# Performance work log

Hardware: AMD Instinct MI355X
Metric: run time of the kernel (lower is better)

The kernel has to match this reference:

```python
import jax, jax.numpy as jnp
import numpy as np

HIDDEN = 64

def setup_inputs() -> dict:
    key = jax.random.key(0)
    ks = jax.random.split(key, 9)
    B, C, H, W = 32, 64, 64, 64
    h = HIDDEN
    s = 0.05
    return {
        "inputs": jax.random.normal(ks[0], (B, C, H, W), jnp.float32),
        # 1x1 Conv2d input->4h gates, stored as [4h, C]
        "w_i2s": jax.random.normal(ks[1], (4 * h, C), jnp.float32) * s,
        "b_i2s": jax.random.normal(ks[2], (4 * h,), jnp.float32) * s,
        # Conv1d(h, 4h, kernel=2): [4h, h, 2]
        "w_s2s": jax.random.normal(ks[3], (4 * h, h, 2), jnp.float32) * s,
        "b_s2s": jax.random.normal(ks[4], (4 * h,), jnp.float32) * s,
        # Conv1d(h, h, kernel=2): [h, h, 2]
        "w_c2c": jax.random.normal(ks[5], (h, h, 2), jnp.float32) * s,
        "b_c2c": jax.random.normal(ks[6], (h,), jnp.float32) * s,
        # 1x1 Conv2d h->2h upsampling, stored as [2h, h]
        "w_up": jax.random.normal(ks[7], (2 * h, h), jnp.float32) * s,
        "b_up": jax.random.normal(ks[8], (2 * h,), jnp.float32) * s,
    }


def _diagonal_lstm(inputs, w_i2s, b_i2s, w_s2s, b_s2s, w_c2c, b_c2c, w_up, b_up):
    B, C, H, W = inputs.shape
    h = w_s2s.shape[1]
    NW = H + W - 1  # skewed width

    # ---- skew: row r of the image shifted right by r columns ----
    rows = jnp.arange(H)[:, None]          # [H,1]
    cols = rows + jnp.arange(W)[None, :]   # [H,W]
    skewed = jnp.zeros((B, C, H, NW), inputs.dtype).at[:, :, rows, cols].set(inputs)

    # ---- input-to-state 1x1 conv -> [B, 4h, H, NW] ----
    i2s = jnp.einsum('bchw,oc->bohw', skewed, w_i2s) + b_i2s[None, :, None, None]
    # per-step input: [NW, B, H*4h]  (layout (H, 4h) flattened, as in torch)
    rnn_in = jnp.transpose(i2s, (3, 0, 2, 1)).reshape(NW, B, H * 4 * h)

    # conv1d(kernel=2) taps: out[p] = W0 @ state[p-1] + W1 @ state[p] (+bias)
    Ws0, Ws1 = w_s2s[:, :, 0], w_s2s[:, :, 1]
    Wc0, Wc1 = w_c2c[:, :, 0], w_c2c[:, :, 1]

    def step(carry, i2s_t):
        c_prev, h_prev = carry  # each [B, H, h]
        zrow = jnp.zeros((B, 1, h), inputs.dtype)
        h_shift = jnp.concatenate([zrow, h_prev[:, :-1]], axis=1)
        c_shift = jnp.concatenate([zrow, c_prev[:, :-1]], axis=1)
        s2s = (jnp.einsum('bph,oh->bpo', h_shift, Ws0)
               + jnp.einsum('bph,oh->bpo', h_prev, Ws1)
               + b_s2s)                       # [B, H, 4h]
        c2c = (jnp.einsum('bph,oh->bpo', c_shift, Wc0)
               + jnp.einsum('bph,oh->bpo', c_prev, Wc1)
               + b_c2c)                       # [B, H, h]
        lstm = jax.nn.sigmoid(i2s_t + s2s.reshape(B, H * 4 * h))
        ig, gg, fg, og = jnp.split(lstm, 4, axis=1)  # each [B, h*H] (faithful flat split)
        c2c_flat = c2c.reshape(B, H * h)
        c = fg * c2c_flat + ig * gg
        hh = og * jnp.tanh(c)
        new_carry = (c.reshape(B, H, h), hh.reshape(B, H, h))
        return new_carry, hh

    init = (jnp.zeros((B, H, h), inputs.dtype), jnp.zeros((B, H, h), inputs.dtype))
    _, outs = jax.lax.scan(step, init, rnn_in)   # outs: [NW, B, H*h]

    # [NW,B,H*h] -> [B, NW, H, h] -> [B, h, H, NW]
    outs = jnp.transpose(outs, (1, 0, 2)).reshape(B, NW, H, h)
    skewed_out = jnp.transpose(outs, (0, 3, 2, 1))

    # ---- unskew ----
    unskewed = skewed_out[:, :, rows, cols]  # [B, h, H, W]

    # ---- 1x1 upsampling conv h -> 2h ----
    return jnp.einsum('bchw,oc->bohw', unskewed, w_up) + b_up[None, :, None, None]


def reference(inputs, w_i2s, b_i2s, w_s2s, b_s2s, w_c2c, b_c2c, w_up, b_up):
    return _diagonal_lstm(inputs, w_i2s, b_i2s, w_s2s, b_s2s, w_c2c, b_c2c, w_up, b_up)
```

## Files before the change

### kernel.cpp

```cpp
#include <hip/hip_runtime.h>
#include <cstdint>
#include <cstddef>


typedef unsigned int u32;
typedef unsigned short u16;
typedef __bf16 bf16x8 __attribute__((ext_vector_type(8)));
typedef float f32x4 __attribute__((ext_vector_type(4)));

#define NSTEP 127
#define MFMA(a, b, c) __builtin_amdgcn_mfma_f32_16x16x32_bf16(a, b, c, 0, 0, 0)
#define LOG2E 1.4426950408889634f
#define SCL (-1.4426950408889634f)
#define T2L 2.8853900817779268f
#define RHO(r) ((((r) ^ ((r) >> 3))) & 7)

static __device__ __forceinline__ u16 f2bf(float f) {
    u32 u = __builtin_bit_cast(u32, f);
    u32 r = u + 0x7FFFu + ((u >> 16) & 1u);
    return (u16)(r >> 16);
}
static __device__ __forceinline__ u32 pack2(float a, float b) {
    return (u32)f2bf(a) | ((u32)f2bf(b) << 16);
}
static __device__ __forceinline__ float lo2f(u32 u) {
    return __builtin_bit_cast(float, u << 16);
}
static __device__ __forceinline__ float hi2f(u32 u) {
    return __builtin_bit_cast(float, u & 0xFFFF0000u);
}
static __device__ __forceinline__ float sigm2(float y) {
    return __builtin_amdgcn_rcpf(1.f + __builtin_amdgcn_exp2f(y));
}
static __device__ __forceinline__ float tanh_fast(float x) {
    float r = __builtin_amdgcn_rcpf(1.f + __builtin_amdgcn_exp2f(x * T2L));
    return __builtin_fmaf(-2.f, r, 1.f);
}

__global__ __launch_bounds__(256) void repack_w(
    const float* __restrict__ w_s2s, const float* __restrict__ w_c2c,
    const float* __restrict__ bi, const float* __restrict__ bs,
    const float* __restrict__ w_up, float* __restrict__ Wg,
    float* __restrict__ Wc, u16* __restrict__ biasRow,
    u16* __restrict__ w_upB) {
    int idx = blockIdx.x * 256 + threadIdx.x;
    if (idx < 32768) {
        int o = idx >> 7, kk = idx & 127, half = kk >> 6, k = kk & 63;
        Wg[idx] = SCL * w_s2s[(o * 64 + k) * 2 + half];
        return;
    }
    int j = idx - 32768;
    if (j < 8192) {
        int o = j >> 7, kk = j & 127, half = kk >> 6, k = kk & 63;
        Wc[j] = w_c2c[(o * 64 + k) * 2 + half];
        return;
    }
    j -= 8192;
    if (j < 256) {
        int m15 = j >> 4, nq = (j >> 2) & 3, nb = j & 3;
        int o = 64 * nq + 16 * nb + m15;
        biasRow[j] = f2bf(SCL * (bi[o] + bs[o]));
        return;
    }
    j -= 256;
    if (j < 8192) w_upB[j] = f2bf(w_up[j]);
}

__global__ __launch_bounds__(256, 2) void i2s_kernel(
    const float* __restrict__ in, const float* __restrict__ w_i2s,
    const float* __restrict__ bi, const float* __restrict__ bs,
    const u32* __restrict__ biasU32, u32* __restrict__ out_u32) {
    const int bid = blockIdx.x;
    const int b = bid >> 6, r = bid & 63;
    const int tid = threadIdx.x;
    const int lane = tid & 63;
    const int wv = __builtin_amdgcn_readfirstlane(tid >> 6);
    const int m15 = lane & 15, g4 = lane >> 4;

    __shared__ __align__(16) u32 sT[64 * 129];
    __shared__ __align__(16) u32 Xt[64 * 32];
    char* XtB = (char*)Xt;

    {
        const int w = tid & 63, cp = tid >> 6;
        const float* xp = in + (size_t)b * 262144 + r * 64 + w;
#pragma unroll
        for (int pass = 0; pass < 8; pass++) {
            int c = pass * 8 + cp * 2;
            float x0 = xp[(size_t)c * 4096];
            float x1 = xp[(size_t)(c + 1) * 4096];
            *(u32*)(XtB + ((w * 128 + c * 2) ^ ((w & 7) << 4))) = pack2(x0, x1);
        }
    }

    bf16x8 Af[4][2];
#pragma unroll
    for (int m = 0; m < 4; m++)
#pragma unroll
        for (int kt = 0; kt < 2; kt++) {
            const float* p =
                w_i2s + (wv * 64 + m * 16 + m15) * 64 + kt * 32 + g4 * 8;
            bf16x8 f;
#pragma unroll
            for (int j = 0; j < 8; j++) f[j] = (__bf16)p[j];
            Af[m][kt] = f;
        }
    float bias[4][4];
#pragma unroll
    for (int m = 0; m < 4; m++)
#pragma unroll
        for (int reg = 0; reg < 4; reg++) {
            int o = wv * 64 + m * 16 + 4 * g4 + reg;
            bias[m][reg] = bi[o] + bs[o];
        }

    __syncthreads();

    f32x4 acc[4][4] = {};
#pragma unroll
    for (int nt = 0; nt < 4; nt++) {
        const int w = nt * 16 + m15;
        bf16x8 Bf[2];
#pragma unroll
        for (int kt = 0; kt < 2; kt++)
            Bf[kt] = __builtin_bit_cast(
                bf16x8, *(const uint4*)(XtB + ((w * 128 + kt * 64 + g4 * 16) ^
                                               ((w & 7) << 4))));
#pragma unroll
        for (int m = 0; m < 4; m++)
#pragma unroll
            for (int kt = 0; kt < 2; kt++)
                acc[m][nt] = MFMA(Af[m][kt], Bf[kt], acc[m][nt]);
    }

#pragma unroll
    for (int nt = 0; nt < 4; nt++) {
        const int w = nt * 16 + m15;
#pragma unroll
        for (int reg = 0; reg < 4; reg++)
#pragma unroll
            for (int mp = 0; mp < 2; mp++) {
                float v0 = SCL * (acc[2 * mp][nt][reg] + bias[2 * mp][reg]);
                float v1 =
                    SCL * (acc[2 * mp + 1][nt][reg] + bias[2 * mp + 1][reg]);
                sT[w * 129 + (4 * g4 + reg) * 8 + wv * 2 + mp] = pack2(v0, v1);
            }
    }
    __syncthreads();

    const size_t base = ((size_t)(b * 64 + r) * 66 + 1) * 128;
#pragma unroll
    for (int loop = 0; loop < 32; loop++) {
        int idx = loop * 256 + tid;
        int w = idx >> 7, cu = idx & 127;
        out_u32[base + idx] = sT[w * 129 + cu];
    }
    if (tid < 128) {
        u32 v = biasU32[tid];
        out_u32[base - 128 + tid] = v;
        out_u32[base + 8192 + tid] = v;
    }
}

__global__ __launch_bounds__(512, 2) void scan_kernel(
    const u16* __restrict__ i2sP, const float* __restrict__ Wg,
    const float* __restrict__ Wc, const float* __restrict__ b_c2c,
    u16* __restrict__ hh16) {
    const int b = blockIdx.x;
    const int tid = threadIdx.x;
    const int lane = tid & 63;
    const int wv = __builtin_amdgcn_readfirstlane(tid >> 6);
    const int mh = wv >> 2, nq = wv & 3;
    const int mtc = wv >> 1, ktc0 = (wv & 1) * 2;
    const int m15 = lane & 15, g4 = lane >> 4;

    __shared__ __align__(16) u32 sM[10304];
    __shared__ __align__(16) u32 sCCm[2048];
    char* smB = (char*)sM;
    char* ccB = (char*)sCCm;

    for (int i = tid; i < 10304; i += 512) sM[i] = 0;

    bf16x8 BW[4][4];
    float bcc[4];
#pragma unroll
    for (int nb = 0; nb < 4; nb++) {
        int o = 64 * nq + 16 * nb + m15;
        bcc[nb] = b_c2c[16 * nb + m15];
#pragma unroll
        for (int kt = 0; kt < 4; kt++) {
            const float* p = Wg + o * 128 + kt * 32 + g4 * 8;
            bf16x8 f;
#pragma unroll
            for (int j = 0; j < 8; j++) f[j] = (__bf16)p[j];
            BW[nb][kt] = f;
        }
    }
    bf16x8 BC[2][4];
#pragma unroll
    for (int i = 0; i < 2; i++) {
        int o2 = 16 * (ktc0 + i) + m15;
#pragma unroll
        for (int kt = 0; kt < 4; kt++) {
            const float* p = Wc + o2 * 128 + kt * 32 + g4 * 8;
            bf16x8 f;
#pragma unroll
            for (int j = 0; j < 8; j++) f[j] = (__bf16)p[j];
            BC[i][kt] = f;
        }
    }

    int aG[2][4], aC[4], wOff[2][4], ccR[2][4], ccP[4], bOffB[2][4];
#pragma unroll
    for (int mi = 0; mi < 2; mi++) {
        int mt = 2 * mh + mi;
#pragma unroll
        for (int kt = 0; kt < 4; kt++) {
            int P = 16 * (m15 & 3) + 4 * mt + (m15 >> 2);
            int phys = P + (kt >> 1) - 1;
            int chunk = (kt & 1) * 4 + g4;
            aG[mi][kt] = (phys < 0) ? (32768 + chunk * 16)
                                    : (phys * 128 + ((chunk ^ RHO(phys)) * 16));
        }
        int p2 = 16 * mt + 4 * g4 + nq;
#pragma unroll
        for (int nb = 0; nb < 4; nb++) {
            int k = 16 * nb + m15;
            wOff[mi][nb] =
                8192 + p2 * 128 + (((k >> 3) ^ RHO(p2)) * 16) + (k & 7) * 2;
            int rp = p2 >> 1;
            ccR[mi][nb] = (rp * 64 + ((k + 8 * rp) & 63)) * 4;
            int prerow = 16 * nb + 4 * mt + g4;
            bOffB[mi][nb] = (prerow * 66 + 1) * 512 + 32 * m15 + 8 * nq;
        }
    }
#pragma unroll
    for (int kt = 0; kt < 4; kt++) {
        int crow = 16 * mtc + m15;
        int phys = crow + (kt >> 1) - 1;
        int chunk = (kt & 1) * 4 + g4;
        aC[kt] = (phys < 0) ? (32896 + chunk * 16)
                            : (16384 + phys * 128 + ((chunk ^ RHO(phys)) * 16));
    }
#pragma unroll
    for (int i = 0; i < 2; i++) {
        int k = 16 * (ktc0 + i) + m15;
        int rp0 = 8 * mtc + 2 * g4, rp1 = rp0 + 1;
        ccP[2 * i] = (rp0 * 64 + ((k + 8 * rp0) & 63)) * 4;
        ccP[2 * i + 1] = (rp1 * 64 + ((k + 8 * rp1) & 63)) * 4;
    }

    const char* i2sB = (const char*)i2sP + (size_t)b * (64 * 66 * 512);
    u16* hp16[2];
    int p2s[2];
#pragma unroll
    for (int mi = 0; mi < 2; mi++) {
        int p2 = 16 * (2 * mh + mi) + 4 * g4 + nq;
        p2s[mi] = p2;
        hp16[mi] = hh16 + (size_t)b * 262144 + p2 * 4032 + m15;
    }

    uint2 IV[2][4];
#pragma unroll
    for (int mi = 0; mi < 2; mi++) {
        int mt = 2 * mh + mi;
#pragma unroll
        for (int r = 0; r < 4; r++) {
            int prerow = 16 * r + 4 * mt + g4;
            int w = min(max(0 - prerow, -1), 64);
            IV[mi][r] = *(const uint2*)(i2sB + (bOffB[mi][r] + (w << 9)));
        }
    }

    u16 hbKeep[2][4];
    u16* hpPrev[2];
    bool vstPrev[2];
#pragma unroll
    for (int mi = 0; mi < 2; mi++) {
        vstPrev[mi] = false;
        hpPrev[mi] = hp16[mi];
    }

    __syncthreads();

    for (int t = 0; t < NSTEP; t++) {
#pragma unroll
        for (int mi = 0; mi < 2; mi++)
            if (vstPrev[mi]) {
#pragma unroll
                for (int nb = 0; nb < 4; nb++)
                    hpPrev[mi][nb * 16] = hbKeep[mi][nb];
            }

        uint2 IVn[2][4];
#pragma unroll
        for (int mi = 0; mi < 2; mi++) {
            int mt = 2 * mh + mi;
#pragma unroll
            for (int r = 0; r < 4; r++) {
                int prerow = 16 * r + 4 * mt + g4;
                int w = min(max(t + 1 - prerow, -1), 64);
                IVn[mi][r] = *(const uint2*)(i2sB + (bOffB[mi][r] + (w << 9)));
            }
        }

        f32x4 accG[2][4];
#pragma unroll
        for (int mi = 0; mi < 2; mi++) {
#pragma unroll
            for (int r = 0; r < 4; r++) {
                accG[mi][0][r] = lo2f(IV[mi][r].x);
                accG[mi][1][r] = hi2f(IV[mi][r].x);
                accG[mi][2][r] = lo2f(IV[mi][r].y);
                accG[mi][3][r] = hi2f(IV[mi][r].y);
            }
            bf16x8 Ag[4];
#pragma unroll
            for (int kt = 0; kt < 4; kt++)
                Ag[kt] = __builtin_bit_cast(bf16x8,
                                            *(const uint4*)(smB + aG[mi][kt]));
#pragma unroll
            for (int nb = 0; nb < 4; nb++)
#pragma unroll
                for (int kt = 0; kt < 4; kt++)
                    accG[mi][nb] = MFMA(Ag[kt], BW[nb][kt], accG[mi][nb]);
        }
        f32x4 accC[2] = {};
        {
            bf16x8 Ac[4];
#pragma unroll
            for (int kt = 0; kt < 4; kt++)
                Ac[kt] =
                    __builtin_bit_cast(bf16x8, *(const uint4*)(smB + aC[kt]));
#pragma unroll
            for (int i = 0; i < 2; i++)
#pragma unroll
                for (int kt = 0; kt < 4; kt++)
                    accC[i] = MFMA(Ac[kt], BC[i][kt], accC[i]);
        }

#pragma unroll
        for (int i = 0; i < 2; i++) {
            *(u32*)(ccB + ccP[2 * i]) = pack2(accC[i][0], accC[i][1]);
            *(u32*)(ccB + ccP[2 * i + 1]) = pack2(accC[i][2], accC[i][3]);
        }
        __syncthreads();

#pragma unroll
        for (int mi = 0; mi < 2; mi++) {
            int p2 = p2s[mi];
            bool vst = (u32)(t - p2) < 64u;
#pragma unroll
            for (int nb = 0; nb < 4; nb++) {
                u32 cw = *(const u32*)(ccB + ccR[mi][nb]);
                float cc = ((nq & 1) ? hi2f(cw) : lo2f(cw)) + bcc[nb];
                float si = sigm2(accG[mi][nb][0]);
                float sg = sigm2(accG[mi][nb][1]);
                float sf = sigm2(accG[mi][nb][2]);
                float so = sigm2(accG[mi][nb][3]);
                float c1 = __builtin_fmaf(sf, cc, si * sg);
                float h1 = so * tanh_fast(c1);
                u16 hb = f2bf(h1);
                *(u16*)(smB + wOff[mi][nb]) = hb;
                *(u16*)(smB + wOff[mi][nb] + 16384) = f2bf(c1);
                hbKeep[mi][nb] = hb;
            }
            vstPrev[mi] = vst;
            hpPrev[mi] = hp16[mi];
            hp16[mi] += 64;
        }
        __syncthreads();

#pragma unroll
        for (int mi = 0; mi < 2; mi++) {
#pragma unroll
            for (int r = 0; r < 4; r++) IV[mi][r] = IVn[mi][r];
#pragma unroll
            for (int kt = 0; kt < 4; kt++) aG[mi][kt] ^= 8192;
#pragma unroll
            for (int nb = 0; nb < 4; nb++) wOff[mi][nb] ^= 8192;
        }
#pragma unroll
        for (int kt = 0; kt < 4; kt++) aC[kt] ^= 8192;
    }

#pragma unroll
    for (int mi = 0; mi < 2; mi++)
        if (vstPrev[mi]) {
#pragma unroll
            for (int nb = 0; nb < 4; nb++)
                hpPrev[mi][nb * 16] = hbKeep[mi][nb];
        }
}

__global__ __launch_bounds__(256) void up_kernel(
    const u16* __restrict__ hh16, const u16* __restrict__ w_upB,
    const float* __restrict__ b_up, float* __restrict__ out) {
    const int bid = blockIdx.x;
    const int b = bid >> 6, r = bid & 63;
    const int lane = threadIdx.x & 63;
    const int wt = __builtin_amdgcn_readfirstlane(threadIdx.x >> 6);
    const int m15 = lane & 15, g4 = lane >> 4;

    const u16* hh_b = hh16 + (size_t)b * 262144;
    const int w = 16 * wt + m15;

    bf16x8 Bf[2];
#pragma unroll
    for (int kt = 0; kt < 2; kt++)
        Bf[kt] = __builtin_bit_cast(
            bf16x8,
            *(const uint4*)(hh_b + (r * 4096 + w * 64 + kt * 32 + g4 * 8)));

    f32x4 acc[8] = {};
#pragma unroll
    for (int nt = 0; nt < 8; nt++) {
#pragma unroll
        for (int kt = 0; kt < 2; kt++) {
            bf16x8 Af = __builtin_bit_cast(
                bf16x8, *(const uint4*)(w_upB + ((16 * nt + m15) * 64 +
                                                 kt * 32 + g4 * 8)));
            acc[nt] = MFMA(Af, Bf[kt], acc[nt]);
        }
    }
    float* outb = out + (size_t)b * 524288;
#pragma unroll
    for (int nt = 0; nt < 8; nt++) {
#pragma unroll
        for (int rr = 0; rr < 4; rr++) {
            int o2 = 16 * nt + 4 * g4 + rr;
            outb[(size_t)o2 * 4096 + r * 64 + w] = acc[nt][rr] + b_up[o2];
        }
    }
}

extern "C" void kernel_launch(void* const* d_in, const int* in_sizes, int n_in,
                              void* d_out, int out_size, void* d_ws,
                              size_t ws_size, hipStream_t stream) {
    (void)in_sizes; (void)n_in; (void)out_size; (void)ws_size;
    const float* inputs = (const float*)d_in[0];
    const float* w_i2s = (const float*)d_in[1];
    const float* b_i2s = (const float*)d_in[2];
    const float* w_s2s = (const float*)d_in[3];
    const float* b_s2s = (const float*)d_in[4];
    const float* w_c2c = (const float*)d_in[5];
    const float* b_c2c = (const float*)d_in[6];
    const float* w_up = (const float*)d_in[7];
    const float* b_up = (const float*)d_in[8];
    float* out = (float*)d_out;
    char* ws = (char*)d_ws;

    u16* i2sP = (u16*)ws;
    u16* hh16 = (u16*)(ws + 69206016);
    float* Wg = (float*)(ws + 85983232);
    float* Wc = (float*)(ws + 86114304);
    u16* biasRow = (u16*)(ws + 86147072);
    u16* w_upB = (u16*)(ws + 86147584);

    hipLaunchKernelGGL(repack_w, dim3(193), dim3(256), 0, stream, w_s2s, w_c2c,
                       b_i2s, b_s2s, w_up, Wg, Wc, biasRow, w_upB);
    hipLaunchKernelGGL(i2s_kernel, dim3(2048), dim3(256), 0, stream, inputs,
                       w_i2s, b_i2s, b_s2s, (const u32*)biasRow, (u32*)i2sP);
    hipLaunchKernelGGL(scan_kernel, dim3(32), dim3(512), 0, stream, i2sP, Wg,
                       Wc, b_c2c, hh16);
    hipLaunchKernelGGL(up_kernel, dim3(2048), dim3(256), 0, stream, hh16,
                       w_upB, b_up, out);
}
```

Measured before the change: 444.7 us.

## Compute c2c conv redundantly per wave to drop shared-memory exchange and barrier

```diff
diff --git a/kernel.cpp b/kernel.cpp
--- a/kernel.cpp
+++ b/kernel.cpp
@@ -171,13 +171,10 @@
     const int lane = tid & 63;
     const int wv = __builtin_amdgcn_readfirstlane(tid >> 6);
     const int mh = wv >> 2, nq = wv & 3;
-    const int mtc = wv >> 1, ktc0 = (wv & 1) * 2;
     const int m15 = lane & 15, g4 = lane >> 4;
 
     __shared__ __align__(16) u32 sM[10304];
-    __shared__ __align__(16) u32 sCCm[2048];
     char* smB = (char*)sM;
-    char* ccB = (char*)sCCm;
 
     for (int i = tid; i < 10304; i += 512) sM[i] = 0;
 
@@ -196,21 +193,21 @@
             BW[nb][kt] = f;
         }
     }
-    bf16x8 BC[2][4];
-#pragma unroll
-    for (int i = 0; i < 2; i++) {
-        int o2 = 16 * (ktc0 + i) + m15;
+    bf16x8 BC[4][4];
+#pragma unroll
+    for (int nb = 0; nb < 4; nb++) {
+        int o2 = 16 * nb + m15;
 #pragma unroll
         for (int kt = 0; kt < 4; kt++) {
             const float* p = Wc + o2 * 128 + kt * 32 + g4 * 8;
             bf16x8 f;
 #pragma unroll
             for (int j = 0; j < 8; j++) f[j] = (__bf16)p[j];
-            BC[i][kt] = f;
-        }
-    }
-
-    int aG[2][4], aC[4], wOff[2][4], ccR[2][4], ccP[4], bOffB[2][4];
+            BC[nb][kt] = f;
+        }
+    }
+
+    int aG[2][4], aC[2][4], wOff[2][4], bOffB[2][4];
 #pragma unroll
     for (int mi = 0; mi < 2; mi++) {
         int mt = 2 * mh + mi;
@@ -221,6 +218,12 @@
             int chunk = (kt & 1) * 4 + g4;
             aG[mi][kt] = (phys < 0) ? (32768 + chunk * 16)
                                     : (phys * 128 + ((chunk ^ RHO(phys)) * 16));
+            int crow = 16 * mt + ((m15 & 12) | ((m15 + nq) & 3));
+            int cphys = crow + (kt >> 1) - 1;
+            aC[mi][kt] = (cphys < 0)
+                             ? (32896 + chunk * 16)
+                             : (16384 + cphys * 128 +
+                                ((chunk ^ RHO(cphys)) * 16));
         }
         int p2 = 16 * mt + 4 * g4 + nq;
 #pragma unroll
@@ -228,26 +231,9 @@
             int k = 16 * nb + m15;
             wOff[mi][nb] =
                 8192 + p2 * 128 + (((k >> 3) ^ RHO(p2)) * 16) + (k & 7) * 2;
-            int rp = p2 >> 1;
-            ccR[mi][nb] = (rp * 64 + ((k + 8 * rp) & 63)) * 4;
             int prerow = 16 * nb + 4 * mt + g4;
             bOffB[mi][nb] = (prerow * 66 + 1) * 512 + 32 * m15 + 8 * nq;
         }
-    }
-#pragma unroll
-    for (int kt = 0; kt < 4; kt++) {
-        int crow = 16 * mtc + m15;
-        int phys = crow + (kt >> 1) - 1;
-        int chunk = (kt & 1) * 4 + g4;
-        aC[kt] = (phys < 0) ? (32896 + chunk * 16)
-                            : (16384 + phys * 128 + ((chunk ^ RHO(phys)) * 16));
-    }
-#pragma unroll
-    for (int i = 0; i < 2; i++) {
-        int k = 16 * (ktc0 + i) + m15;
-        int rp0 = 8 * mtc + 2 * g4, rp1 = rp0 + 1;
-        ccP[2 * i] = (rp0 * 64 + ((k + 8 * rp0) & 63)) * 4;
-        ccP[2 * i + 1] = (rp1 * 64 + ((k + 8 * rp1) & 63)) * 4;
     }
 
     const char* i2sB = (const char*)i2sP + (size_t)b * (64 * 66 * 512);
@@ -292,27 +278,25 @@
                     hpPrev[mi][nb * 16] = hbKeep[mi][nb];
             }
 
-        uint2 IVn[2][4];
 #pragma unroll
         for (int mi = 0; mi < 2; mi++) {
             int mt = 2 * mh + mi;
+
+            uint2 tn[4];
 #pragma unroll
             for (int r = 0; r < 4; r++) {
                 int prerow = 16 * r + 4 * mt + g4;
                 int w = min(max(t + 1 - prerow, -1), 64);
-                IVn[mi][r] = *(const uint2*)(i2sB + (bOffB[mi][r] + (w << 9)));
-            }
-        }
-
-        f32x4 accG[2][4];
-#pragma unroll
-        for (int mi = 0; mi < 2; mi++) {
+                tn[r] = *(const uint2*)(i2sB + (bOffB[mi][r] + (w << 9)));
+            }
+
+            f32x4 accG[4];
 #pragma unroll
             for (int r = 0; r < 4; r++) {
-                accG[mi][0][r] = lo2f(IV[mi][r].x);
-                accG[mi][1][r] = hi2f(IV[mi][r].x);
-                accG[mi][2][r] = lo2f(IV[mi][r].y);
-                accG[mi][3][r] = hi2f(IV[mi][r].y);
+                accG[0][r] = lo2f(IV[mi][r].x);
+                accG[1][r] = hi2f(IV[mi][r].x);
+                accG[2][r] = lo2f(IV[mi][r].y);
+                accG[3][r] = hi2f(IV[mi][r].y);
             }
             bf16x8 Ag[4];
 #pragma unroll
@@ -323,41 +307,31 @@
             for (int nb = 0; nb < 4; nb++)
 #pragma unroll
                 for (int kt = 0; kt < 4; kt++)
-                    accG[mi][nb] = MFMA(Ag[kt], BW[nb][kt], accG[mi][nb]);
-        }
-        f32x4 accC[2] = {};
-        {
-            bf16x8 Ac[4];
-#pragma unroll
-            for (int kt = 0; kt < 4; kt++)
-                Ac[kt] =
-                    __builtin_bit_cast(bf16x8, *(const uint4*)(smB + aC[kt]));
-#pragma unroll
-            for (int i = 0; i < 2; i++)
+                    accG[nb] = MFMA(Ag[kt], BW[nb][kt], accG[nb]);
+
+            f32x4 accC[4] = {};
+            {
+                bf16x8 Ac[4];
 #pragma unroll
                 for (int kt = 0; kt < 4; kt++)
-                    accC[i] = MFMA(Ac[kt], BC[i][kt], accC[i]);
-        }
-
-#pragma unroll
-        for (int i = 0; i < 2; i++) {
-            *(u32*)(ccB + ccP[2 * i]) = pack2(accC[i][0], accC[i][1]);
-            *(u32*)(ccB + ccP[2 * i + 1]) = pack2(accC[i][2], accC[i][3]);
-        }
-        __syncthreads();
-
-#pragma unroll
-        for (int mi = 0; mi < 2; mi++) {
+                    Ac[kt] = __builtin_bit_cast(
+                        bf16x8, *(const uint4*)(smB + aC[mi][kt]));
+#pragma unroll
+                for (int nb = 0; nb < 4; nb++)
+#pragma unroll
+                    for (int kt = 0; kt < 4; kt++)
+                        accC[nb] = MFMA(Ac[kt], BC[nb][kt], accC[nb]);
+            }
+
             int p2 = p2s[mi];
             bool vst = (u32)(t - p2) < 64u;
 #pragma unroll
             for (int nb = 0; nb < 4; nb++) {
-                u32 cw = *(const u32*)(ccB + ccR[mi][nb]);
-                float cc = ((nq & 1) ? hi2f(cw) : lo2f(cw)) + bcc[nb];
-                float si = sigm2(accG[mi][nb][0]);
-                float sg = sigm2(accG[mi][nb][1]);
-                float sf = sigm2(accG[mi][nb][2]);
-                float so = sigm2(accG[mi][nb][3]);
+                float cc = accC[nb][0] + bcc[nb];
+                float si = sigm2(accG[nb][0]);
+                float sg = sigm2(accG[nb][1]);
+                float sf = sigm2(accG[nb][2]);
+                float so = sigm2(accG[nb][3]);
                 float c1 = __builtin_fmaf(sf, cc, si * sg);
                 float h1 = so * tanh_fast(c1);
                 u16 hb = f2bf(h1);
@@ -368,20 +342,23 @@
             vstPrev[mi] = vst;
             hpPrev[mi] = hp16[mi];
             hp16[mi] += 64;
-        }
+
+#pragma unroll
+            for (int r = 0; r < 4; r++) IV[mi][r] = tn[r];
+        }
+
         __syncthreads();
 
 #pragma unroll
         for (int mi = 0; mi < 2; mi++) {
 #pragma unroll
-            for (int r = 0; r < 4; r++) IV[mi][r] = IVn[mi][r];
-#pragma unroll
-            for (int kt = 0; kt < 4; kt++) aG[mi][kt] ^= 8192;
+            for (int kt = 0; kt < 4; kt++) {
+                aG[mi][kt] ^= 8192;
+                aC[mi][kt] ^= 8192;
+            }
 #pragma unroll
             for (int nb = 0; nb < 4; nb++) wOff[mi][nb] ^= 8192;
         }
-#pragma unroll
-        for (int kt = 0; kt < 4; kt++) aC[kt] ^= 8192;
     }
 
 #pragma unroll
```

After: 436.0 us. About the same (-1.9%).
